# Kernel optimization log

Measured on AMD Instinct MI355X. Metric: run time of the kernel, lower is better.

## Reference

```python
import jax, jax.numpy as jnp
import numpy as np

D_MODEL = 256
N_HEADS = 8
B, S = 8, 2048
TEMP = jnp.sqrt(jnp.float32(D_MODEL))  # ScaledDotProductAttention(temperature=d_model) -> sqrt(d_model)
NEG = jnp.float32(-1e9)


def setup_inputs() -> dict:
    key = jax.random.key(0)
    ks = jax.random.split(key, 12)
    dh = D_MODEL * N_HEADS
    sc_in = 1.0 / np.sqrt(D_MODEL)
    sc_out = 1.0 / np.sqrt(dh)
    return {
        "query": jax.random.normal(ks[0], (B, S, D_MODEL), jnp.float32),
        "key": jax.random.normal(ks[1], (B, S, D_MODEL), jnp.float32),
        "value": jax.random.normal(ks[2], (B, S, D_MODEL), jnp.float32),
        "mask": jax.random.bernoulli(ks[3], 0.9, (B, S)),
        "Wq": jax.random.normal(ks[4], (D_MODEL, dh), jnp.float32) * sc_in,
        "bq": jnp.zeros((dh,), jnp.float32),
        "Wk": jax.random.normal(ks[5], (D_MODEL, dh), jnp.float32) * sc_in,
        "bk": jnp.zeros((dh,), jnp.float32),
        "Wv": jax.random.normal(ks[6], (D_MODEL, dh), jnp.float32) * sc_in,
        "bv": jnp.zeros((dh,), jnp.float32),
        "Wo": jax.random.normal(ks[7], (dh, D_MODEL), jnp.float32) * sc_out,
        "bo": jnp.zeros((D_MODEL,), jnp.float32),
    }


def reference(query, key, value, mask, Wq, bq, Wk, bk, Wv, bv, Wo, bo):
    nb = query.shape[0]
    # projections: (B,S,d) @ (d, d*H) -> view (B,S,H,d)
    q = (query @ Wq + bq).reshape(nb, -1, N_HEADS, D_MODEL)
    k = (key @ Wk + bk).reshape(nb, -1, N_HEADS, D_MODEL)
    v = (value @ Wv + bv).reshape(nb, -1, N_HEADS, D_MODEL)
    # torch.matmul on (B,S,H,d): batched over (B,S) -> per-position HxH attention
    attn = jnp.einsum('bshd,bsgd->bshg', q, k) / TEMP
    m = mask[:, :, None, None]  # (B,S,1,1) broadcast, as in mask.view(B,-1,1,1)
    attn = jnp.where(m, attn, NEG)
    attn = jax.nn.softmax(attn, axis=-1)  # dropout p=0 -> identity
    x = jnp.einsum('bshg,bsgd->bshd', attn, v)  # (B,S,H,d)
    # x.transpose(1,2).contiguous().view(B,-1,d*H)
    x = jnp.transpose(x, (0, 2, 1, 3)).reshape(nb, -1, D_MODEL * N_HEADS)
    return x @ Wo + bo
```

## Files before the change

### kernel.cpp

```cpp
#include <hip/hip_runtime.h>
#include <hip/hip_bf16.h>

typedef __hip_bfloat16 bf16;
typedef short bf16x8 __attribute__((ext_vector_type(8)));
typedef float f32x4 __attribute__((ext_vector_type(4)));

#define MFMA16(a,b,c) __builtin_amdgcn_mfma_f32_16x16x32_bf16(a,b,c,0,0,0)

__device__ __forceinline__ unsigned short f2us(float x){
    union{__hip_bfloat16 h; unsigned short u;} c; c.h = __float2bfloat16(x); return c.u;
}
__device__ __forceinline__ float us2f(unsigned short u){
    union{unsigned short u; __hip_bfloat16 h;} c; c.u = u; return __bfloat162float(c.h);
}
__device__ __forceinline__ uint4 pack8(float4 a, float4 b){
    union{unsigned short us[8]; uint4 v;} p;
    p.us[0]=f2us(a.x); p.us[1]=f2us(a.y); p.us[2]=f2us(a.z); p.us[3]=f2us(a.w);
    p.us[4]=f2us(b.x); p.us[5]=f2us(b.y); p.us[6]=f2us(b.z); p.us[7]=f2us(b.w);
    return p.v;
}

__global__ __launch_bounds__(256) void prep_kernel(
    const float* __restrict__ Wq, const float* __restrict__ Wk,
    const float* __restrict__ Wv, const float* __restrict__ bq,
    const float* __restrict__ bk, const float* __restrict__ bv,
    const float* __restrict__ Wo,
    bf16* __restrict__ WqT, bf16* __restrict__ WkT, bf16* __restrict__ WvT,
    float* __restrict__ bqp, float* __restrict__ bkp, float* __restrict__ bvp,
    bf16* __restrict__ WoT)
{
    __shared__ float T[64][68];
    const int tid = threadIdx.x, bx = blockIdx.x;
    if (bx < 384) {
        const int mat = bx / 128, rem = bx % 128;
        const int c0 = (rem >> 5) * 64, n0 = (rem & 31) * 64;
        const float* W = (mat == 0) ? Wq : (mat == 1) ? Wk : Wv;
        bf16* WT = (mat == 0) ? WqT : (mat == 1) ? WkT : WvT;
        #pragma unroll
        for (int it = 0; it < 4; ++it) {
            int pp = tid + (it << 8);
            int cl = pp >> 4, n4 = (pp & 15) * 4;
            float4 f = *(const float4*)(W + (size_t)(c0 + cl) * 2048 + n0 + n4);
            T[cl][n4] = f.x; T[cl][n4+1] = f.y; T[cl][n4+2] = f.z; T[cl][n4+3] = f.w;
        }
        __syncthreads();
        const int h = n0 >> 8, d0 = n0 & 255;
        #pragma unroll
        for (int it = 0; it < 2; ++it) {
            int pp = tid + (it << 8);
            int j = pp >> 3, g = pp & 7;
            union{unsigned short us[8]; uint4 v;} pk;
            #pragma unroll
            for (int u = 0; u < 8; ++u) pk.us[u] = f2us(T[g*8+u][j]);
            *(uint4*)(WT + (size_t)((d0 + j) * 8 + h) * 256 + c0 + g * 8) = pk.v;
        }
    } else if (bx < 387) {
        const int mat = bx - 384;
        const float* src = (mat == 0) ? bq : (mat == 1) ? bk : bv;
        float* dst = (mat == 0) ? bqp : (mat == 1) ? bkp : bvp;
        for (int n = tid; n < 2048; n += 256)
            dst[(n & 255) * 8 + (n >> 8)] = src[n];
    } else {
        const int idx = bx - 387;
        const int k0 = (idx >> 2) * 64, c0 = (idx & 3) * 64;
        #pragma unroll
        for (int it = 0; it < 4; ++it) {
            int pp = tid + (it << 8);
            int kl = pp >> 4, c4 = (pp & 15) * 4;
            float4 f = *(const float4*)(Wo + (size_t)(k0 + kl) * 256 + c0 + c4);
            T[kl][c4] = f.x; T[kl][c4+1] = f.y; T[kl][c4+2] = f.z; T[kl][c4+3] = f.w;
        }
        __syncthreads();
        #pragma unroll
        for (int it = 0; it < 2; ++it) {
            int pp = tid + (it << 8);
            int j = pp >> 3, g = pp & 7;
            union{unsigned short us[8]; uint4 v;} pk;
            #pragma unroll
            for (int u = 0; u < 8; ++u) pk.us[u] = f2us(T[g*8+u][j]);
            *(uint4*)(WoT + (size_t)(c0 + j) * 2048 + k0 + g * 8) = pk.v;
        }
    }
}

__global__ __launch_bounds__(512, 2) void qk_kernel(
    const float* __restrict__ Qin, const float* __restrict__ Kin,
    const int* __restrict__ mask,
    const bf16* __restrict__ WqT, const bf16* __restrict__ WkT,
    const float* __restrict__ bqp, const float* __restrict__ bkp,
    float* __restrict__ w)
{
    __shared__ __align__(16) char smem[147456];
    char* const Xq = smem;
    char* const Xk = smem + 32768;
    char* const QT = smem + 65536;
    char* const KT = smem + 106496;
    float* const RED = (float*)smem;

    const int tid  = threadIdx.x;
    const int wid  = tid >> 6, lane = tid & 63;
    const int quad = lane >> 4, l15 = lane & 15;
    const int tok0 = blockIdx.x * 64;

    #pragma unroll
    for (int it = 0; it < 4; ++it) {
        int pp = tid + (it << 9);
        int row = pp >> 5, g = pp & 31;
        const float* s = Qin + (size_t)(tok0 + row) * 256 + g * 8;
        *(uint4*)(Xq + row * 512 + ((g ^ (row & 7)) << 4)) =
            pack8(*(const float4*)s, *(const float4*)(s + 4));
        s = Kin + (size_t)(tok0 + row) * 256 + g * 8;
        *(uint4*)(Xk + row * 512 + ((g ^ (row & 7)) << 4)) =
            pack8(*(const float4*)s, *(const float4*)(s + 4));
    }
    __syncthreads();

    f32x4 sacc[4];
    #pragma unroll
    for (int p = 0; p < 4; ++p)
        #pragma unroll
        for (int i = 0; i < 4; ++i) sacc[p][i] = 0.f;

    for (int Cp = 0; Cp < 8; ++Cp) {
        f32x4 accq[4][2], acck[4][2];
        #pragma unroll
        for (int mt = 0; mt < 4; ++mt)
            #pragma unroll
            for (int nt = 0; nt < 2; ++nt)
                #pragma unroll
                for (int i = 0; i < 4; ++i) { accq[mt][nt][i] = 0.f; acck[mt][nt][i] = 0.f; }
        #pragma unroll
        for (int Ks = 0; Ks < 8; ++Ks) {
            bf16x8 bq[2], bk[2];
            #pragma unroll
            for (int nt = 0; nt < 2; ++nt) {
                const size_t boff =
                    (size_t)(Cp * 256 + wid * 32 + nt * 16 + l15) * 256 + Ks * 32 + quad * 8;
                bq[nt] = *(const bf16x8*)(WqT + boff);
                bk[nt] = *(const bf16x8*)(WkT + boff);
            }
            #pragma unroll
            for (int mt = 0; mt < 4; ++mt) {
                int row = mt * 16 + l15;
                int G = (Ks * 4 + quad) ^ (row & 7);
                bf16x8 aq = *(const bf16x8*)(Xq + row * 512 + (G << 4));
                bf16x8 ak = *(const bf16x8*)(Xk + row * 512 + (G << 4));
                #pragma unroll
                for (int nt = 0; nt < 2; ++nt) {
                    accq[mt][nt] = MFMA16(aq, bq[nt], accq[mt][nt]);
                    acck[mt][nt] = MFMA16(ak, bk[nt], acck[mt][nt]);
                }
            }
        }
        #pragma unroll
        for (int nt = 0; nt < 2; ++nt) {
            const int p2 = wid * 32 + nt * 16 + l15;
            const int rowoff = p2 * 160 + ((p2 >> 6) & 3) * 8;
            const float biq = bqp[Cp * 256 + p2];
            const float bik = bkp[Cp * 256 + p2];
            #pragma unroll
            for (int mt = 0; mt < 4; ++mt) {
                int t0 = mt * 16 + quad * 4;
                union{unsigned short us[4]; uint2 v;} pq, pk;
                #pragma unroll
                for (int i = 0; i < 4; ++i) {
                    pq.us[i] = f2us(accq[mt][nt][i] + biq);
                    pk.us[i] = f2us(acck[mt][nt][i] + bik);
                }
                *(uint2*)(QT + rowoff + t0 * 2) = pq.v;
                *(uint2*)(KT + rowoff + t0 * 2) = pk.v;
            }
        }
        __syncthreads();
        #pragma unroll
        for (int pp2 = 0; pp2 < 4; ++pp2) {
            int tq = 2 * (wid * 4 + pp2) + (l15 >> 3);
            union{unsigned short us[8]; bf16x8 v;} Aq, Bk;
            #pragma unroll
            for (int j = 0; j < 8; ++j) {
                int p2 = (quad * 8 + j) * 8 + (l15 & 7);
                int off = p2 * 160 + ((p2 >> 6) & 3) * 8 + tq * 2;
                Aq.us[j] = *(const unsigned short*)(QT + off);
                Bk.us[j] = *(const unsigned short*)(KT + off);
            }
            sacc[pp2] = MFMA16(Aq.v, Bk.v, sacc[pp2]);
        }
        __syncthreads();
    }

    if ((quad >> 1) == (l15 >> 3)) {
        #pragma unroll
        for (int pp2 = 0; pp2 < 4; ++pp2) {
            int tl = (wid * 4 + pp2) * 2 + (l15 >> 3);
            #pragma unroll
            for (int i = 0; i < 4; ++i)
                RED[tl * 68 + ((quad & 1) * 4 + i) * 8 + (l15 & 7)] = sacc[pp2][i];
        }
    }
    __syncthreads();
    {
        const int tl = tid >> 3, hh = tid & 7;
        const int mk = mask[tok0 + tl];
        const float* r = RED + tl * 68 + hh * 8;
        float m = r[0];
        #pragma unroll
        for (int g = 1; g < 8; ++g) m = fmaxf(m, r[g]);
        float e[8], sum = 0.f;
        #pragma unroll
        for (int g = 0; g < 8; ++g) { e[g] = __expf((r[g] - m) * 0.0625f); sum += e[g]; }
        float inv = 1.f / sum;
        float o[8];
        #pragma unroll
        for (int g = 0; g < 8; ++g) o[g] = mk ? e[g] * inv : 0.125f;
        float* wp = w + (size_t)(tok0 + tl) * 64 + hh * 8;
        *(float4*)wp = make_float4(o[0], o[1], o[2], o[3]);
        *(float4*)(wp + 4) = make_float4(o[4], o[5], o[6], o[7]);
    }
}

__global__ __launch_bounds__(512, 2) void av_kernel(
    const float* __restrict__ Vin,
    const bf16* __restrict__ WvT, const float* __restrict__ bvp,
    const float* __restrict__ w, const bf16* __restrict__ WoT,
    const float* __restrict__ bo, float* __restrict__ Out)
{
    __shared__ __align__(16) char smem[100352];
    char* const Xv  = smem;
    char* const VT0 = smem + 32768;
    char* const VT1 = smem + 50176;
    char* const xS0 = smem + 67584;
    char* const xS1 = smem + 83968;

    const int tid  = threadIdx.x;
    const int wid  = tid >> 6, lane = tid & 63;
    const int quad = lane >> 4, l15 = lane & 15;
    const int tok0 = blockIdx.x * 64;
    const int t6   = tid & 63, dg = tid >> 6;

    #pragma unroll
    for (int it = 0; it < 4; ++it) {
        int pp = tid + (it << 9);
        int row = pp >> 5, g = pp & 31;
        const float* s = Vin + (size_t)(tok0 + row) * 256 + g * 8;
        *(uint4*)(Xv + row * 512 + ((g ^ (row & 7)) << 4)) =
            pack8(*(const float4*)s, *(const float4*)(s + 4));
    }
    float wv[64];
    {
        const float* wp = w + (size_t)(tok0 + t6) * 64;
        #pragma unroll
        for (int i = 0; i < 16; ++i) {
            float4 f = ((const float4*)wp)[i];
            wv[i*4] = f.x; wv[i*4+1] = f.y; wv[i*4+2] = f.z; wv[i*4+3] = f.w;
        }
    }
    __syncthreads();

    const int pll = wid * 16 + l15;

    f32x4 oacc[4][2];
    #pragma unroll
    for (int mt = 0; mt < 4; ++mt)
        #pragma unroll
        for (int nt = 0; nt < 2; ++nt)
            #pragma unroll
            for (int i = 0; i < 4; ++i) oacc[mt][nt][i] = 0.f;

    for (int p = 0; p < 18; ++p) {
        char* const VTw = (p & 1) ? VT1 : VT0;
        char* const VTr = (p & 1) ? VT0 : VT1;
        char* const xSw = (p & 1) ? xS0 : xS1;
        char* const xSr = (p & 1) ? xS1 : xS0;

        if (p < 16) {
            const int C = p;
            f32x4 acc[4];
            #pragma unroll
            for (int mt = 0; mt < 4; ++mt)
                #pragma unroll
                for (int i = 0; i < 4; ++i) acc[mt][i] = 0.f;
            #pragma unroll
            for (int Ks = 0; Ks < 8; ++Ks) {
                bf16x8 b = *(const bf16x8*)(WvT + (size_t)(C * 128 + pll) * 256 + Ks * 32 + quad * 8);
                #pragma unroll
                for (int mt = 0; mt < 4; ++mt) {
                    int row = mt * 16 + l15;
                    int G = (Ks * 4 + quad) ^ (row & 7);
                    bf16x8 a = *(const bf16x8*)(Xv + row * 512 + (G << 4));
                    acc[mt] = MFMA16(a, b, acc[mt]);
                }
            }
            const float biv = bvp[C * 128 + pll];
            #pragma unroll
            for (int mt = 0; mt < 4; ++mt) {
                int t0 = mt * 16 + quad * 4;
                union{unsigned short us[4]; uint2 v;} pk;
                #pragma unroll
                for (int i = 0; i < 4; ++i) pk.us[i] = f2us(acc[mt][i] + biv);
                *(uint2*)(VTw + pll * 136 + t0 * 2) = pk.v;
            }
        }

        if (p >= 1 && p <= 16) {
            #pragma unroll
            for (int dd = 0; dd < 2; ++dd) {
                int d = dg * 2 + dd;
                float vv[8];
                #pragma unroll
                for (int g = 0; g < 8; ++g)
                    vv[g] = us2f(*(const unsigned short*)(VTr + (d * 8 + g) * 136 + t6 * 2));
                #pragma unroll
                for (int h = 0; h < 8; ++h) {
                    float x = 0.f;
                    #pragma unroll
                    for (int g = 0; g < 8; ++g) x = fmaf(wv[h * 8 + g], vv[g], x);
                    int u = (h * 2 + (d >> 3)) ^ (t6 & 15);
                    *(unsigned short*)(xSw + t6 * 256 + u * 16 + (d & 7) * 2) = f2us(x);
                }
            }
        }

        if (p >= 2) {
            const int C = p - 2;
            #pragma unroll
            for (int m = 0; m < 4; ++m) {
                const int j  = 2 * m + (quad >> 1);
                const int k0 = j * 256 + C * 16 + (quad & 1) * 8;
                bf16x8 bfr[2];
                #pragma unroll
                for (int nt = 0; nt < 2; ++nt) {
                    int c = wid * 32 + nt * 16 + l15;
                    bfr[nt] = *(const bf16x8*)(WoT + (size_t)c * 2048 + k0);
                }
                #pragma unroll
                for (int mt = 0; mt < 4; ++mt) {
                    int h = mt * 2 + (l15 >> 3);
                    int t = (l15 & 7) * 8 + j;
                    int u = (h * 2 + (quad & 1)) ^ (t & 15);
                    bf16x8 afr = *(const bf16x8*)(xSr + t * 256 + u * 16);
                    #pragma unroll
                    for (int nt = 0; nt < 2; ++nt)
                        oacc[mt][nt] = MFMA16(afr, bfr[nt], oacc[mt][nt]);
                }
            }
        }

        __syncthreads();
    }

    const int b = tok0 >> 11, sg0 = (tok0 & 2047) >> 3;
    #pragma unroll
    for (int nt = 0; nt < 2; ++nt) {
        int c = wid * 32 + nt * 16 + l15;
        float bias = bo[c];
        #pragma unroll
        for (int mt = 0; mt < 4; ++mt) {
            #pragma unroll
            for (int i = 0; i < 4; ++i) {
                int rr = mt * 16 + quad * 4 + i;
                int h = rr >> 3, sgl = rr & 7;
                size_t r = ((size_t)b << 11) + h * 256 + sg0 + sgl;
                Out[r * 256 + c] = oacc[mt][nt][i] + bias;
            }
        }
    }
}

extern "C" void kernel_launch(void* const* d_in, const int* in_sizes, int n_in,
                              void* d_out, int out_size, void* d_ws, size_t ws_size,
                              hipStream_t stream) {
    const float* query = (const float*)d_in[0];
    const float* key   = (const float*)d_in[1];
    const float* value = (const float*)d_in[2];
    const int*   mask  = (const int*)  d_in[3];
    const float* Wq = (const float*)d_in[4];  const float* bq = (const float*)d_in[5];
    const float* Wk = (const float*)d_in[6];  const float* bk = (const float*)d_in[7];
    const float* Wv = (const float*)d_in[8];  const float* bv = (const float*)d_in[9];
    const float* Wo = (const float*)d_in[10]; const float* bo = (const float*)d_in[11];

    char* ws = (char*)d_ws;
    bf16*  WoT = (bf16*)ws;
    bf16*  WqT = (bf16*)(ws + 1048576);
    bf16*  WkT = (bf16*)(ws + 2097152);
    bf16*  WvT = (bf16*)(ws + 3145728);
    float* bqp = (float*)(ws + 4194304);
    float* bkp = (float*)(ws + 4202496);
    float* bvp = (float*)(ws + 4210688);
    float* w   = (float*)(ws + 4218880);

    prep_kernel<<<515, 256, 0, stream>>>(
        Wq, Wk, Wv, bq, bk, bv, Wo, WqT, WkT, WvT, bqp, bkp, bvp, WoT);
    qk_kernel<<<256, 512, 0, stream>>>(
        query, key, mask, WqT, WkT, bqp, bkp, w);
    av_kernel<<<256, 512, 0, stream>>>(
        value, WvT, bvp, w, WoT, bo, (float*)d_out);
}
```

Baseline: 268.8 us.

## Fuse QK softmax and AV/output projection kernels into one kernel

Merges the qk kernel and the av kernel into a single kernel. The per-token 8x8 attention weights are passed through LDS instead of a global workspace round trip. This removes one kernel launch and the global write and read of the weight tensor. In exchange the fused kernel carries the larger 147KB LDS footprint through the AV phase and serialises the V load after softmax, which may reduce occupancy and overlap.

```diff
diff --git a/kernel.cpp b/kernel.cpp
--- a/kernel.cpp
+++ b/kernel.cpp
@@ -83,24 +83,34 @@
     }
 }
 
-__global__ __launch_bounds__(512, 2) void qk_kernel(
+__global__ __launch_bounds__(512, 2) void qkav_kernel(
     const float* __restrict__ Qin, const float* __restrict__ Kin,
-    const int* __restrict__ mask,
+    const float* __restrict__ Vin, const int* __restrict__ mask,
     const bf16* __restrict__ WqT, const bf16* __restrict__ WkT,
+    const bf16* __restrict__ WvT,
     const float* __restrict__ bqp, const float* __restrict__ bkp,
-    float* __restrict__ w)
+    const float* __restrict__ bvp,
+    const bf16* __restrict__ WoT, const float* __restrict__ bo,
+    float* __restrict__ Out)
 {
     __shared__ __align__(16) char smem[147456];
     char* const Xq = smem;
     char* const Xk = smem + 32768;
     char* const QT = smem + 65536;
     char* const KT = smem + 106496;
-    float* const RED = (float*)smem;
+    float* const RED  = (float*)smem;
+    float* const WLDS = (float*)(smem + 106496);
+    char* const Xv  = smem;
+    char* const VT0 = smem + 32768;
+    char* const VT1 = smem + 50176;
+    char* const xS0 = smem + 67584;
+    char* const xS1 = smem + 83968;
 
     const int tid  = threadIdx.x;
     const int wid  = tid >> 6, lane = tid & 63;
     const int quad = lane >> 4, l15 = lane & 15;
     const int tok0 = blockIdx.x * 64;
+    const int t6   = tid & 63, dg = tid >> 6;
 
     #pragma unroll
     for (int it = 0; it < 4; ++it) {
@@ -212,31 +222,21 @@
         float o[8];
         #pragma unroll
         for (int g = 0; g < 8; ++g) o[g] = mk ? e[g] * inv : 0.125f;
-        float* wp = w + (size_t)(tok0 + tl) * 64 + hh * 8;
+        float* wp = WLDS + tl * 68 + hh * 8;
         *(float4*)wp = make_float4(o[0], o[1], o[2], o[3]);
         *(float4*)(wp + 4) = make_float4(o[4], o[5], o[6], o[7]);
     }
-}
-
-__global__ __launch_bounds__(512, 2) void av_kernel(
-    const float* __restrict__ Vin,
-    const bf16* __restrict__ WvT, const float* __restrict__ bvp,
-    const float* __restrict__ w, const bf16* __restrict__ WoT,
-    const float* __restrict__ bo, float* __restrict__ Out)
-{
-    __shared__ __align__(16) char smem[100352];
-    char* const Xv  = smem;
-    char* const VT0 = smem + 32768;
-    char* const VT1 = smem + 50176;
-    char* const xS0 = smem + 67584;
-    char* const xS1 = smem + 83968;
-
-    const int tid  = threadIdx.x;
-    const int wid  = tid >> 6, lane = tid & 63;
-    const int quad = lane >> 4, l15 = lane & 15;
-    const int tok0 = blockIdx.x * 64;
-    const int t6   = tid & 63, dg = tid >> 6;
-
+    __syncthreads();
+
+    float wv[64];
+    {
+        const float* wl = WLDS + t6 * 68;
+        #pragma unroll
+        for (int i = 0; i < 16; ++i) {
+            float4 f = *(const float4*)(wl + i * 4);
+            wv[i*4] = f.x; wv[i*4+1] = f.y; wv[i*4+2] = f.z; wv[i*4+3] = f.w;
+        }
+    }
     #pragma unroll
     for (int it = 0; it < 4; ++it) {
         int pp = tid + (it << 9);
@@ -244,15 +244,6 @@
         const float* s = Vin + (size_t)(tok0 + row) * 256 + g * 8;
         *(uint4*)(Xv + row * 512 + ((g ^ (row & 7)) << 4)) =
             pack8(*(const float4*)s, *(const float4*)(s + 4));
-    }
-    float wv[64];
-    {
-        const float* wp = w + (size_t)(tok0 + t6) * 64;
-        #pragma unroll
-        for (int i = 0; i < 16; ++i) {
-            float4 f = ((const float4*)wp)[i];
-            wv[i*4] = f.x; wv[i*4+1] = f.y; wv[i*4+2] = f.z; wv[i*4+3] = f.w;
-        }
     }
     __syncthreads();
 
@@ -386,12 +377,10 @@
     float* bqp = (float*)(ws + 4194304);
     float* bkp = (float*)(ws + 4202496);
     float* bvp = (float*)(ws + 4210688);
-    float* w   = (float*)(ws + 4218880);
 
     prep_kernel<<<515, 256, 0, stream>>>(
         Wq, Wk, Wv, bq, bk, bv, Wo, WqT, WkT, WvT, bqp, bkp, bvp, WoT);
-    qk_kernel<<<256, 512, 0, stream>>>(
-        query, key, mask, WqT, WkT, bqp, bkp, w);
-    av_kernel<<<256, 512, 0, stream>>>(
-        value, WvT, bvp, w, WoT, bo, (float*)d_out);
-}
+    qkav_kernel<<<256, 512, 0, stream>>>(
+        query, key, value, mask, WqT, WkT, WvT, bqp, bkp, bvp, WoT, bo,
+        (float*)d_out);
+}
```

Result: faster. 262.7 us (-2.3%).
